# Performance work log

Hardware: AMD Instinct MI355X
Metric: run time of the kernel (lower is better)

Reference implementation:

```python
import jax, jax.numpy as jnp
import numpy as np

FEATURE_DIM = 256
KEEP = 64  # low-frequency block size kept after the pseudo-DCT


def setup_inputs() -> dict:
    key = jax.random.key(0)
    k_x, k_w, k_b = jax.random.split(key, 3)
    B, C, H, W = 32, 3, 512, 512
    x = jax.random.uniform(k_x, (B, C, H, W), dtype=jnp.float32)
    # nn.Linear(64*64, feature_dim): weight [out, in], bias [out]
    fan_in = KEEP * KEEP
    bound = 1.0 / np.sqrt(fan_in)
    fc_w = jax.random.uniform(k_w, (FEATURE_DIM, fan_in), dtype=jnp.float32, minval=-bound, maxval=bound)
    fc_b = jax.random.uniform(k_b, (FEATURE_DIM,), dtype=jnp.float32, minval=-bound, maxval=bound)
    return {"x": x, "fc_w": fc_w, "fc_b": fc_b}


def reference(x, fc_w, fc_b):
    # grayscale conversion (input has 3 channels)
    x_gray = 0.299 * x[:, 0] + 0.587 * x[:, 1] + 0.114 * x[:, 2]  # [B, H, W]
    # "dct2d": FFT along last dim, then FFT along second-to-last, real part
    X = jnp.fft.fft(jnp.fft.fft(x_gray, axis=-1), axis=-2).real  # [B, H, W]
    # keep low-frequency 64x64 block and flatten
    coeffs = X[:, :KEEP, :KEEP].reshape(x.shape[0], KEEP * KEEP)  # [B, 4096]
    # final linear projection
    return coeffs @ fc_w.T + fc_b  # [B, feature_dim]
```

## Files before the change

kernel.cpp:

```cpp
#include <hip/hip_runtime.h>

#define HW_ (512 * 512)
#define TWOPI_512 0.01227184630308513f

typedef __attribute__((ext_vector_type(8))) _Float16 half8;
typedef __attribute__((ext_vector_type(4))) _Float16 half4;
typedef __attribute__((ext_vector_type(4))) float    f32x4;

template<bool SIN>
__device__ __forceinline__ void k1_loop(const _Float16 (*g)[520],
                                        int l15, int quad, int mk0, int mk1,
                                        f32x4& acc0, f32x4& acc1)
{
    float c0r[8], s0r[8], c1r[8], s1r[8];
#pragma unroll
    for (int j = 0; j < 8; ++j) {
        float a0 = (float)((mk0 * j) & 511) * TWOPI_512;
        float a1 = (float)((mk1 * j) & 511) * TWOPI_512;
        c0r[j] = __cosf(a0); s0r[j] = __sinf(a0);
        c1r[j] = __cosf(a1); s1r[j] = __sinf(a1);
    }
    for (int k0 = 0; k0 < 512; k0 += 32) {
        int kc = k0 + quad * 8;
        half8 bv = *(const half8*)&g[l15][kc];
        float b0 = (float)((mk0 * kc) & 511) * TWOPI_512;
        float b1 = (float)((mk1 * kc) & 511) * TWOPI_512;
        float cb0 = __cosf(b0), sb0 = __sinf(b0);
        float cb1 = __cosf(b1), sb1 = __sinf(b1);
        half8 a0v, a1v;
#pragma unroll
        for (int j = 0; j < 8; ++j) {
            float v0 = SIN ? (sb0 * c0r[j] + cb0 * s0r[j])
                           : (cb0 * c0r[j] - sb0 * s0r[j]);
            float v1 = SIN ? (sb1 * c1r[j] + cb1 * s1r[j])
                           : (cb1 * c1r[j] - sb1 * s1r[j]);
            a0v[j] = (_Float16)v0;
            a1v[j] = (_Float16)v1;
        }
        acc0 = __builtin_amdgcn_mfma_f32_16x16x32_f16(a0v, bv, acc0, 0, 0, 0);
        acc1 = __builtin_amdgcn_mfma_f32_16x16x32_f16(a1v, bv, acc1, 0, 0, 0);
    }
}

__global__ __launch_bounds__(256) void k1(const float* __restrict__ x,
                                          const float* __restrict__ fc_w,
                                          _Float16* __restrict__ PF,
                                          _Float16* __restrict__ whF)
{
    __shared__ _Float16 g[16][520];
    int t = threadIdx.x;

    if (blockIdx.x == 32) {
        int pid = blockIdx.y;
        for (int it = 0; it < 16; ++it) {
            int idx8 = pid * 4096 + it * 256 + t;
            int lane = idx8 & 63;
            int f = ((idx8 >> 6) & 15) * 16 + (lane & 15);
            int k = (idx8 >> 10) * 32 + ((lane >> 4) << 3);
            const float* wp = fc_w + (size_t)f * 4096 + k;
            float4 f0 = *(const float4*)wp;
            float4 f1 = *(const float4*)(wp + 4);
            half8 o;
            o[0] = (_Float16)(f0.x * 16.0f);
            o[1] = (_Float16)(f0.y * 16.0f);
            o[2] = (_Float16)(f0.z * 16.0f);
            o[3] = (_Float16)(f0.w * 16.0f);
            o[4] = (_Float16)(f1.x * 16.0f);
            o[5] = (_Float16)(f1.y * 16.0f);
            o[6] = (_Float16)(f1.z * 16.0f);
            o[7] = (_Float16)(f1.w * 16.0f);
            *(half8*)(whF + (size_t)idx8 * 8) = o;
        }
        return;
    }

    int h0 = blockIdx.x * 16;
    int b  = blockIdx.y;
    const float* xb = x + (size_t)b * 3 * HW_;

    for (int i = 0; i < 8; ++i) {
        int slot = t + i * 256;
        int hh = slot >> 7, w4 = slot & 127;
        const float* p = xb + (size_t)(h0 + hh) * 512 + w4 * 4;
        float4 r  = *(const float4*)p;
        float4 gg = *(const float4*)(p + HW_);
        float4 bb = *(const float4*)(p + 2 * HW_);
        half4 o;
        o.x = (_Float16)(0.299f * r.x + 0.587f * gg.x + 0.114f * bb.x);
        o.y = (_Float16)(0.299f * r.y + 0.587f * gg.y + 0.114f * bb.y);
        o.z = (_Float16)(0.299f * r.z + 0.587f * gg.z + 0.114f * bb.z);
        o.w = (_Float16)(0.299f * r.w + 0.587f * gg.w + 0.114f * bb.w);
        *(half4*)&g[hh][w4 * 4] = o;
    }
    __syncthreads();

    int lane = t & 63, wv = t >> 6, l15 = lane & 15, quad = lane >> 4;
    int mk0 = (wv * 32 + l15) & 63;
    int mk1 = (wv * 32 + 16 + l15) & 63;

    f32x4 acc[2];
    acc[0] = (f32x4){0.f, 0.f, 0.f, 0.f};
    acc[1] = (f32x4){0.f, 0.f, 0.f, 0.f};

    if (wv >= 2) k1_loop<true >(g, l15, quad, mk0, mk1, acc[0], acc[1]);
    else         k1_loop<false>(g, l15, quad, mk0, mk1, acc[0], acc[1]);

    _Float16* Pb = PF + (size_t)b * 65536;
    int h = h0 + l15;
    for (int mi = 0; mi < 2; ++mi)
        for (int r = 0; r < 4; ++r) {
            int m = wv * 32 + mi * 16 + quad * 4 + r;
            float v = acc[mi][r];
            int m64 = m & 63;
            int tt  = (m < 64) ? (h >> 5) : 16 + (h >> 5);
            if (m >= 64) v = -v;
            int lp = (m64 & 15) | (((h >> 3) & 3) << 4);
            Pb[(size_t)((tt * 4 + (m64 >> 4)) * 64 + lp) * 8 + (h & 7)] = (_Float16)v;
        }
}

template<bool SIN>
__device__ __forceinline__ void k2_loop(const _Float16* __restrict__ Pb,
                                        int t0, int kh, int quad, int lane,
                                        f32x4* acc)
{
    for (int it = 0; it < 8; ++it) {
        int tt = t0 + it;
        int kgb = tt * 32 + quad * 8;
        half8 a;
#pragma unroll
        for (int j = 0; j < 8; ++j) {
            int h = (kgb + j) & 511;
            float ang = (float)(__mul24(kh, h) & 511) * TWOPI_512;
            a[j] = (_Float16)(SIN ? __sinf(ang) : __cosf(ang));
        }
        for (int ni = 0; ni < 4; ++ni) {
            half8 bv = *(const half8*)(Pb + (size_t)((tt * 4 + ni) * 64 + lane) * 8);
            acc[ni] = __builtin_amdgcn_mfma_f32_16x16x32_f16(a, bv, acc[ni], 0, 0, 0);
        }
    }
}

__global__ __launch_bounds__(256) void k2(const _Float16* __restrict__ PF,
                                          _Float16* __restrict__ XF)
{
    __shared__ float red[3][64][17];
    int b  = blockIdx.y;
    int bx = blockIdx.x;
    int lane = threadIdx.x & 63, wv = threadIdx.x >> 6;
    int l15 = lane & 15, quad = lane >> 4;
    int kh = bx * 16 + l15;

    const _Float16* Pb = PF + (size_t)b * 65536;
    f32x4 acc[4];
    for (int i = 0; i < 4; ++i) acc[i] = (f32x4){0.f, 0.f, 0.f, 0.f};

    if (wv >= 2) k2_loop<true >(Pb, wv * 8, kh, quad, lane, acc);
    else         k2_loop<false>(Pb, wv * 8, kh, quad, lane, acc);

    if (wv)
        for (int ni = 0; ni < 4; ++ni)
            for (int r = 0; r < 4; ++r)
                red[wv - 1][lane][ni * 4 + r] = acc[ni][r];
    __syncthreads();
    if (!wv)
        for (int ni = 0; ni < 4; ++ni)
            for (int r = 0; r < 4; ++r) {
                float v = acc[ni][r] + red[0][lane][ni * 4 + r]
                                     + red[1][lane][ni * 4 + r]
                                     + red[2][lane][ni * 4 + r];
                int khr = bx * 16 + quad * 4 + r;
                int kw  = ni * 16 + l15;
                int k   = khr * 64 + kw;
                int lp  = (b & 15) | (((k >> 3) & 3) << 4);
                XF[(size_t)(((k >> 5) * 2 + (b >> 4)) * 64 + lp) * 8 + (k & 7)] =
                    (_Float16)(v * 0.0625f);
            }
}

__global__ __launch_bounds__(512) void k3(const _Float16* __restrict__ XF,
                                          const _Float16* __restrict__ whF,
                                          float* __restrict__ wsP)
{
    __shared__ float red[8][64][9];
    int nb = blockIdx.x & 15;
    int kc = blockIdx.x >> 4;
    int tid = threadIdx.x;
    int lane = tid & 63, wv = tid >> 6;

    f32x4 acc[2];
    acc[0] = (f32x4){0.f, 0.f, 0.f, 0.f};
    acc[1] = (f32x4){0.f, 0.f, 0.f, 0.f};

    for (int it = 0; it < 2; ++it) {
        int tt = kc * 16 + wv * 2 + it;
        half8 a0 = *(const half8*)(XF + (size_t)((tt * 2 + 0) * 64 + lane) * 8);
        half8 a1 = *(const half8*)(XF + (size_t)((tt * 2 + 1) * 64 + lane) * 8);
        half8 bv = *(const half8*)(whF + (size_t)((tt * 16 + nb) * 64 + lane) * 8);
        acc[0] = __builtin_amdgcn_mfma_f32_16x16x32_f16(a0, bv, acc[0], 0, 0, 0);
        acc[1] = __builtin_amdgcn_mfma_f32_16x16x32_f16(a1, bv, acc[1], 0, 0, 0);
    }

    for (int j = 0; j < 8; ++j)
        red[wv][lane][j] = acc[j >> 2][j & 3];
    __syncthreads();

    int lp = tid >> 3, j = tid & 7;
    float s = 0.f;
    for (int w = 0; w < 8; ++w) s += red[w][lp][j];
    int batch = (j >> 2) * 16 + (lp >> 4) * 4 + (j & 3);
    int fi = lp & 15;
    wsP[(size_t)blockIdx.x * 512 + batch * 16 + fi] = s;
}

__global__ __launch_bounds__(256) void k4(const float* __restrict__ wsP,
                                          const float* __restrict__ fc_b,
                                          float* __restrict__ out)
{
    int gid = blockIdx.x * 256 + threadIdx.x;
    int m = gid >> 8, f = gid & 255;
    int nb = f >> 4, fi = f & 15;
    float s = fc_b[f];
    for (int kc = 0; kc < 8; ++kc)
        s += wsP[(size_t)(kc * 16 + nb) * 512 + m * 16 + fi];
    out[gid] = s;
}

extern "C" void kernel_launch(void* const* d_in, const int* in_sizes, int n_in,
                              void* d_out, int out_size, void* d_ws, size_t ws_size,
                              hipStream_t stream) {
    const float* x    = (const float*)d_in[0];
    const float* fc_w = (const float*)d_in[1];
    const float* fc_b = (const float*)d_in[2];
    float* out = (float*)d_out;

    char* ws = (char*)d_ws;
    _Float16* PF  = (_Float16*)(ws);
    _Float16* XF  = (_Float16*)(ws + 4194304);
    _Float16* whF = (_Float16*)(ws + 4456448);
    float*    wsP = (float*)   (ws + 6553600);

    k1<<<dim3(33, 32), 256, 0, stream>>>(x, fc_w, PF, whF);
    k2<<<dim3(4, 32),  256, 0, stream>>>(PF, XF);
    k3<<<128, 512, 0, stream>>>(XF, whF, wsP);
    k4<<<32, 256, 0, stream>>>(wsP, fc_b, out);
}
```

Baseline: 162.6 us.

## Fuse final GEMM reduction and bias into k3, drop k4 split-K pass

The GEMM kernel previously split K into 8 chunks across 128 blocks and wrote partials to workspace, with a separate kernel summing them and adding bias. Now each of 32 blocks covers the full K for one batch half and one feature tile, reduces across waves in shared memory, and writes the output with bias directly. This removes one kernel launch and the workspace round trip, in exchange for fewer blocks and longer per-wave MFMA chains.

```diff
diff --git a/kernel.cpp b/kernel.cpp
--- a/kernel.cpp
+++ b/kernel.cpp
@@ -180,50 +180,36 @@
 
 __global__ __launch_bounds__(512) void k3(const _Float16* __restrict__ XF,
                                           const _Float16* __restrict__ whF,
-                                          float* __restrict__ wsP)
-{
-    __shared__ float red[8][64][9];
+                                          const float* __restrict__ fc_b,
+                                          float* __restrict__ out)
+{
+    __shared__ float red[8][64][5];
     int nb = blockIdx.x & 15;
-    int kc = blockIdx.x >> 4;
+    int bt = blockIdx.x >> 4;
     int tid = threadIdx.x;
     int lane = tid & 63, wv = tid >> 6;
 
-    f32x4 acc[2];
-    acc[0] = (f32x4){0.f, 0.f, 0.f, 0.f};
-    acc[1] = (f32x4){0.f, 0.f, 0.f, 0.f};
-
-    for (int it = 0; it < 2; ++it) {
-        int tt = kc * 16 + wv * 2 + it;
-        half8 a0 = *(const half8*)(XF + (size_t)((tt * 2 + 0) * 64 + lane) * 8);
-        half8 a1 = *(const half8*)(XF + (size_t)((tt * 2 + 1) * 64 + lane) * 8);
+    f32x4 acc = (f32x4){0.f, 0.f, 0.f, 0.f};
+
+    for (int it = 0; it < 16; ++it) {
+        int tt = wv * 16 + it;
+        half8 a  = *(const half8*)(XF  + (size_t)((tt * 2 + bt) * 64 + lane) * 8);
         half8 bv = *(const half8*)(whF + (size_t)((tt * 16 + nb) * 64 + lane) * 8);
-        acc[0] = __builtin_amdgcn_mfma_f32_16x16x32_f16(a0, bv, acc[0], 0, 0, 0);
-        acc[1] = __builtin_amdgcn_mfma_f32_16x16x32_f16(a1, bv, acc[1], 0, 0, 0);
-    }
-
-    for (int j = 0; j < 8; ++j)
-        red[wv][lane][j] = acc[j >> 2][j & 3];
+        acc = __builtin_amdgcn_mfma_f32_16x16x32_f16(a, bv, acc, 0, 0, 0);
+    }
+
+    for (int r = 0; r < 4; ++r)
+        red[wv][lane][r] = acc[r];
     __syncthreads();
 
-    int lp = tid >> 3, j = tid & 7;
-    float s = 0.f;
-    for (int w = 0; w < 8; ++w) s += red[w][lp][j];
-    int batch = (j >> 2) * 16 + (lp >> 4) * 4 + (j & 3);
-    int fi = lp & 15;
-    wsP[(size_t)blockIdx.x * 512 + batch * 16 + fi] = s;
-}
-
-__global__ __launch_bounds__(256) void k4(const float* __restrict__ wsP,
-                                          const float* __restrict__ fc_b,
-                                          float* __restrict__ out)
-{
-    int gid = blockIdx.x * 256 + threadIdx.x;
-    int m = gid >> 8, f = gid & 255;
-    int nb = f >> 4, fi = f & 15;
-    float s = fc_b[f];
-    for (int kc = 0; kc < 8; ++kc)
-        s += wsP[(size_t)(kc * 16 + nb) * 512 + m * 16 + fi];
-    out[gid] = s;
+    if (tid < 256) {
+        int lane2 = tid & 63, r = tid >> 6;
+        float s = 0.f;
+        for (int w = 0; w < 8; ++w) s += red[w][lane2][r];
+        int batch = bt * 16 + ((lane2 >> 4) << 2) + r;
+        int f = nb * 16 + (lane2 & 15);
+        out[batch * 256 + f] = s + fc_b[f];
+    }
 }
 
 extern "C" void kernel_launch(void* const* d_in, const int* in_sizes, int n_in,
@@ -238,10 +224,8 @@
     _Float16* PF  = (_Float16*)(ws);
     _Float16* XF  = (_Float16*)(ws + 4194304);
     _Float16* whF = (_Float16*)(ws + 4456448);
-    float*    wsP = (float*)   (ws + 6553600);
 
     k1<<<dim3(33, 32), 256, 0, stream>>>(x, fc_w, PF, whF);
     k2<<<dim3(4, 32),  256, 0, stream>>>(PF, XF);
-    k3<<<128, 512, 0, stream>>>(XF, whF, wsP);
-    k4<<<32, 256, 0, stream>>>(wsP, fc_b, out);
-}
+    k3<<<32, 512, 0, stream>>>(XF, whF, fc_b, out);
+}
```

Result: no change. 162.5 us (-0.0%).
